# Optimization experiments

Measured on AMD Instinct MI355X. Metric: run time of the kernel, lower is better.

The kernel has to match this reference:

```python
import jax, jax.numpy as jnp
import numpy as np

DT = 0.1
THRESH = 0.01


def setup_inputs() -> dict:
    key = jax.random.key(0)
    ks = jax.random.split(key, 4)
    B, C, H, W = 4, 64, 128, 128
    field = jax.random.normal(ks[0], (B, C, H, W), dtype=jnp.float32)
    # depthwise 3x3 conv weight [C,1,3,3], fan_in = 9
    dw = jax.random.normal(ks[1], (C, 1, 3, 3), dtype=jnp.float32) * (1.0 / 3.0)
    db = jnp.zeros((C,), jnp.float32)
    # 1x1 convs as matrices: w1 [2C, C], w2 [C, 2C]
    w1 = jax.random.normal(ks[2], (2 * C, C), dtype=jnp.float32) * (1.0 / np.sqrt(C))
    b1 = jnp.zeros((2 * C,), jnp.float32)
    w2 = jax.random.normal(ks[3], (C, 2 * C), dtype=jnp.float32) * (1.0 / np.sqrt(2 * C))
    b2 = jnp.zeros((C,), jnp.float32)
    dcoeff = jnp.ones((1,), jnp.float32) * 0.1  # diffusion_coeff init
    return {"field": field, "dw": dw, "db": db, "w1": w1, "b1": b1,
            "w2": w2, "b2": b2, "dcoeff": dcoeff, "max_steps": 50}


def _dynamics(f, dw, db, w1, b1, w2, b2, dcoeff):
    C = f.shape[1]
    diff = jax.lax.conv_general_dilated(
        f, dw, window_strides=(1, 1), padding="SAME",
        feature_group_count=C,
        dimension_numbers=("NCHW", "OIHW", "NCHW")) + db[None, :, None, None]
    h = jax.nn.gelu(jnp.einsum("bchw,oc->bohw", f, w1) + b1[None, :, None, None],
                    approximate=False)
    react = jnp.einsum("bchw,oc->bohw", h, w2) + b2[None, :, None, None]
    return dcoeff[0] * diff + react


def reference(field, dw, db, w1, b1, w2, b2, dcoeff, max_steps):
    def step(carry, _):
        f, done, steps = carry
        deriv = _dynamics(f, dw, db, w1, b1, w2, b2, dcoeff)
        new_f = f + DT * deriv
        change = jnp.mean(jnp.abs(new_f - f))
        f2 = jnp.where(done, f, new_f)          # freeze field once converged
        steps2 = steps + jnp.where(done, 0, 1)  # steps_taken is adaptive
        done2 = done | (change < THRESH)
        return (f2, done2, steps2), None

    init = (field, jnp.asarray(False), jnp.asarray(0, jnp.int32))
    (final_field, _, steps), _ = jax.lax.scan(step, init, None, length=max_steps)
    return final_field, steps
```

## Files before the change

### kernel.cpp

```cpp
#include <hip/hip_runtime.h>
#include <math.h>

#define BATCH 4
#define CCH   64
#define HDIM  128
#define WDIM  128
#define HW    (HDIM * WDIM)
#define NELEM (BATCH * CCH * HW)
#define OCH   128
#define NSTEPS 50
#define NBLK  1024
#define DT 0.1f
#define THRESH 0.01f

typedef short bf16x8 __attribute__((ext_vector_type(8)));
typedef float f32x4  __attribute__((ext_vector_type(4)));

__global__ void init_kernel(double* p0, double* p1, int* stepsvar) {
    int i = blockIdx.x * blockDim.x + threadIdx.x;
    if (i < NBLK) {
        p0[i] = (i == 0) ? 1.0e9 : 0.0;
        p1[i] = 0.0;
    }
    if (i == 0) *stepsvar = 0;
}

__device__ __forceinline__ short f2bf(float x) {
    unsigned u = __float_as_uint(x);
    unsigned r = u + 0x7fff + ((u >> 16) & 1);
    return (short)(r >> 16);
}

__device__ __forceinline__ int pk(float a, float b) {
    return (f2bf(a) & 0xffff) | (((int)f2bf(b)) << 16);
}

__device__ __forceinline__ float bf_lo(int v) { return __int_as_float(v << 16); }
__device__ __forceinline__ float bf_hi(int v) { return __int_as_float(v & 0xffff0000); }

__device__ __forceinline__ float dpp_up1(float v) {
    return __int_as_float(__builtin_amdgcn_update_dpp(
        0, __float_as_int(v), 0x138, 0xf, 0xf, false));
}
__device__ __forceinline__ float dpp_dn1(float v) {
    return __int_as_float(__builtin_amdgcn_update_dpp(
        0, __float_as_int(v), 0x130, 0xf, 0xf, false));
}

__global__ void prep_kernel(const float* __restrict__ w1,
                            const float* __restrict__ w2,
                            short* __restrict__ w1b, short* __restrict__ w2b) {
    int i = blockIdx.x * blockDim.x + threadIdx.x;
    if (i < OCH * CCH) {
        w1b[i] = f2bf(w1[i]);
        w2b[i] = f2bf(w2[i]);
    }
}

__device__ __forceinline__ float gelu_fast(float x) {
    float u  = x * 0.70710678118654752f;
    float au = fabsf(u);
    float t  = __builtin_amdgcn_rcpf(fmaf(0.3275911f, au, 1.0f));
    float p  = fmaf(1.061405429f, t, -1.453152027f);
    p = fmaf(p, t, 1.421413741f);
    p = fmaf(p, t, -0.284496736f);
    p = fmaf(p, t, 0.254829592f);
    p = p * t;
    float ex = __expf(-au * au);
    float e  = fmaf(-p, ex, 1.0f);
    float er = copysignf(e, x);
    return 0.5f * x * (1.0f + er);
}

__global__ __launch_bounds__(256, 4) void step_kernel(
    const float* __restrict__ fin, float* __restrict__ fout,
    const float* __restrict__ dw, const float* __restrict__ db,
    const short* __restrict__ w1b, const float* __restrict__ b1,
    const short* __restrict__ w2b, const float* __restrict__ b2,
    const float* __restrict__ dcoeff,
    const double* __restrict__ pin, double* __restrict__ pout,
    int* __restrict__ stepsvar, int sidx)
{
    const int tid  = threadIdx.x;
    const int lane = tid & 63;
    const int w    = tid >> 6;
    const int quad = (lane >> 4);
    const int lp   = lane & 15;
    const int blk  = blockIdx.x;
    const int xcd  = blk & 7;
    const int idx  = blk >> 3;
    const int y    = xcd * 16 + (idx & 15);
    const int b    = (idx >> 4) & 3;
    const int seg  = idx >> 6;
    const int px0  = seg * 64;
    const int fbase = b * CCH * HW + y * WDIM + px0;

    __shared__ int4   sBf4[64 * 8];
    __shared__ int4   sH4 [64 * 16];
    __shared__ float  sSeam[384];
    __shared__ float  sDw[CCH * 9];
    __shared__ float  sDb[CCH];
    __shared__ double sdred[4];
    __shared__ float  wred[4];
    short* sBf = (short*)sBf4;
    short* sH  = (short*)sH4;
    int*   sRi = (int*)sBf4;

    double ds = pin[tid] + pin[tid + 256] + pin[tid + 512] + pin[tid + 768];
    #pragma unroll
    for (int off = 32; off > 0; off >>= 1) ds += __shfl_down(ds, off, 64);
    if (lane == 0) sdred[w] = ds;

    for (int i = tid; i < CCH * 9; i += 256) sDw[i] = dw[i];
    if (tid < CCH) sDb[tid] = db[tid];

    if (tid < 192) {
        #pragma unroll
        for (int k = 0; k < 2; ++k) {
            int e    = tid * 2 + k;
            int row  = e >> 7;
            int side = (e >> 6) & 1;
            int ch   = e & 63;
            int gy   = y - 1 + row;
            int gx   = px0 + (side ? 64 : -1);
            float v  = 0.0f;
            if (gy >= 0 && gy < HDIM && gx >= 0 && gx < WDIM)
                v = fin[b * CCH * HW + ch * HW + gy * WDIM + gx];
            sSeam[e] = v;
        }
    }

    bf16x8 a1[2][2];
    #pragma unroll
    for (int mt = 0; mt < 2; ++mt)
        #pragma unroll
        for (int kk = 0; kk < 2; ++kk)
            a1[mt][kk] = *(const bf16x8*)(w1b + (w * 32 + mt * 16 + lp) * CCH
                                          + kk * 32 + quad * 8);
    f32x4 b1v[2];
    #pragma unroll
    for (int mt = 0; mt < 2; ++mt)
        b1v[mt] = *(const f32x4*)(b1 + w * 32 + mt * 16 + quad * 4);
    f32x4 b2v = *(const f32x4*)(b2 + w * 16 + quad * 4);

    float f[16];
    {
        #pragma unroll
        for (int i = 0; i < 16; ++i)
            f[i] = fin[fbase + (w * 16 + i) * HW + lane];
        int4 v0, v1;
        v0.x = pk(f[0], f[1]);   v0.y = pk(f[2], f[3]);
        v0.z = pk(f[4], f[5]);   v0.w = pk(f[6], f[7]);
        v1.x = pk(f[8], f[9]);   v1.y = pk(f[10], f[11]);
        v1.z = pk(f[12], f[13]); v1.w = pk(f[14], f[15]);
        int g0 = (w * 2)     ^ (lane & 7);
        int g1 = (w * 2 + 1) ^ (lane & 7);
        sBf4[lane * 8 + g0] = v0;
        sBf4[lane * 8 + g1] = v1;
    }
    __syncthreads();

    {
        double tot = sdred[0] + sdred[1] + sdred[2] + sdred[3];
        if ((float)(tot * (1.0 / (double)NELEM)) < THRESH) {
            if (tid == 0) pout[blk] = pin[blk];
            return;
        }
    }
    if (blk == 0 && tid == 0) *stepsvar = sidx + 1;

    f32x4 acc1[2][4];
    #pragma unroll
    for (int mt = 0; mt < 2; ++mt)
        #pragma unroll
        for (int nt = 0; nt < 4; ++nt)
            acc1[mt][nt] = (f32x4)0.0f;

    #pragma unroll
    for (int kk = 0; kk < 2; ++kk) {
        #pragma unroll
        for (int nt = 0; nt < 4; ++nt) {
            int px = nt * 16 + lp;
            int g  = kk * 4 + quad;
            bf16x8 bfrag = *(const bf16x8*)(sBf + px * 64 + (g ^ (px & 7)) * 8);
            #pragma unroll
            for (int mt = 0; mt < 2; ++mt)
                acc1[mt][nt] = __builtin_amdgcn_mfma_f32_16x16x32_bf16(
                    a1[mt][kk], bfrag, acc1[mt][nt], 0, 0, 0);
        }
    }

    bf16x8 a2[4];
    #pragma unroll
    for (int kk = 0; kk < 4; ++kk)
        a2[kk] = *(const bf16x8*)(w2b + (w * 16 + lp) * OCH + kk * 32 + quad * 8);

    #pragma unroll
    for (int mt = 0; mt < 2; ++mt) {
        #pragma unroll
        for (int nt = 0; nt < 4; ++nt) {
            int px = nt * 16 + lp;
            float h0 = gelu_fast(acc1[mt][nt][0] + b1v[mt][0]);
            float h1 = gelu_fast(acc1[mt][nt][1] + b1v[mt][1]);
            float h2 = gelu_fast(acc1[mt][nt][2] + b1v[mt][2]);
            float h3 = gelu_fast(acc1[mt][nt][3] + b1v[mt][3]);
            int o0  = w * 32 + mt * 16 + quad * 4;
            int g   = o0 >> 3;
            int sub = o0 & 7;
            int gp  = (g & 8) | ((g ^ (px & 7)) & 7);
            int2 hv; hv.x = pk(h0, h1); hv.y = pk(h2, h3);
            *(int2*)(sH + px * 128 + gp * 8 + sub) = hv;
        }
    }

    float hm[16], hp[16];
    {
        const float* fb = fin + fbase + lane;
        if (y > 0) {
            #pragma unroll
            for (int i = 0; i < 16; ++i) hm[i] = fb[(w * 16 + i) * HW - WDIM];
        } else {
            #pragma unroll
            for (int i = 0; i < 16; ++i) hm[i] = 0.0f;
        }
        if (y < HDIM - 1) {
            #pragma unroll
            for (int i = 0; i < 16; ++i) hp[i] = fb[(w * 16 + i) * HW + WDIM];
        } else {
            #pragma unroll
            for (int i = 0; i < 16; ++i) hp[i] = 0.0f;
        }
    }
    __syncthreads();

    f32x4 acc2[4];
    #pragma unroll
    for (int nt = 0; nt < 4; ++nt) acc2[nt] = (f32x4)0.0f;

    #pragma unroll
    for (int kk = 0; kk < 4; ++kk) {
        #pragma unroll
        for (int nt = 0; nt < 4; ++nt) {
            int px = nt * 16 + lp;
            int g  = kk * 4 + quad;
            int gp = (g & 8) | ((g ^ (px & 7)) & 7);
            bf16x8 hfrag = *(const bf16x8*)(sH + px * 128 + gp * 8);
            acc2[nt] = __builtin_amdgcn_mfma_f32_16x16x32_bf16(
                a2[kk], hfrag, acc2[nt], 0, 0, 0);
        }
    }

    #pragma unroll
    for (int nt = 0; nt < 4; ++nt) {
        int px = nt * 16 + lp;
        sRi[(w * 8 + quad * 2 + 0) * 64 + px]
            = pk(acc2[nt][0] + b2v[0], acc2[nt][1] + b2v[1]);
        sRi[(w * 8 + quad * 2 + 1) * 64 + px]
            = pk(acc2[nt][2] + b2v[2], acc2[nt][3] + b2v[3]);
    }
    __syncthreads();

    float react[16];
    #pragma unroll
    for (int ii = 0; ii < 8; ++ii) {
        int v = sRi[(w * 8 + ii) * 64 + lane];
        react[2 * ii]     = bf_lo(v);
        react[2 * ii + 1] = bf_hi(v);
    }

    const float dc = dcoeff[0];
    float csum = 0.0f;

    #pragma unroll
    for (int i = 0; i < 16; ++i) {
        const int c = w * 16 + i;
        const float* wk = sDw + c * 9;
        float vm = hm[i], vc = f[i], vp = hp[i];
        float lm = dpp_up1(vm), lc = dpp_up1(vc), lq = dpp_up1(vp);
        float rm = dpp_dn1(vm), rc = dpp_dn1(vc), rq = dpp_dn1(vp);
        lm = (lane == 0)  ? sSeam[0 * 128 + 0 + c]   : lm;
        lc = (lane == 0)  ? sSeam[1 * 128 + 0 + c]   : lc;
        lq = (lane == 0)  ? sSeam[2 * 128 + 0 + c]   : lq;
        rm = (lane == 63) ? sSeam[0 * 128 + 64 + c]  : rm;
        rc = (lane == 63) ? sSeam[1 * 128 + 64 + c]  : rc;
        rq = (lane == 63) ? sSeam[2 * 128 + 64 + c]  : rq;

        float d = sDb[c];
        d = fmaf(wk[0], lm, d); d = fmaf(wk[1], vm, d); d = fmaf(wk[2], rm, d);
        d = fmaf(wk[3], lc, d); d = fmaf(wk[4], vc, d); d = fmaf(wk[5], rc, d);
        d = fmaf(wk[6], lq, d); d = fmaf(wk[7], vp, d); d = fmaf(wk[8], rq, d);

        float nf = vc + DT * (dc * d + react[i]);
        fout[fbase + c * HW + lane] = nf;
        csum += fabsf(nf - vc);
    }

    float v = csum;
    #pragma unroll
    for (int off = 32; off > 0; off >>= 1) v += __shfl_down(v, off, 64);
    if (lane == 0) wred[w] = v;
    __syncthreads();
    if (tid == 0) {
        pout[blk] = (double)wred[0] + (double)wred[1]
                  + (double)wred[2] + (double)wred[3];
    }
}

__global__ void output_kernel(const float* __restrict__ bufA,
                              float* __restrict__ out,
                              const int* __restrict__ stepsvar)
{
    int i = blockIdx.x * blockDim.x + threadIdx.x;
    int K = *stepsvar;
    bool fromA = (((K - 1) & 1) == 0);
    if (i < NELEM && fromA) out[i] = bufA[i];
    if (i == 0) out[NELEM] = (float)K;
}

extern "C" void kernel_launch(void* const* d_in, const int* in_sizes, int n_in,
                              void* d_out, int out_size, void* d_ws, size_t ws_size,
                              hipStream_t stream)
{
    const float* field  = (const float*)d_in[0];
    const float* dw     = (const float*)d_in[1];
    const float* db     = (const float*)d_in[2];
    const float* w1     = (const float*)d_in[3];
    const float* b1     = (const float*)d_in[4];
    const float* w2     = (const float*)d_in[5];
    const float* b2     = (const float*)d_in[6];
    const float* dcoeff = (const float*)d_in[7];

    float* out = (float*)d_out;

    char* ws = (char*)d_ws;
    float*  bufA = (float*)ws;
    short*  w1b  = (short*)(ws + (size_t)NELEM * 4 + 256);
    short*  w2b  = (short*)(ws + (size_t)NELEM * 4 + 256 + 16384);
    double* P0   = (double*)(ws + (size_t)NELEM * 4 + 256 + 32768);
    double* P1   = P0 + NBLK;
    int* stepsvar = (int*)(P1 + NBLK);

    init_kernel<<<4, 256, 0, stream>>>(P0, P1, stepsvar);
    prep_kernel<<<(OCH * CCH + 255) / 256, 256, 0, stream>>>(w1, w2, w1b, w2b);

    float*  bufs[2]  = { bufA, out };
    double* psums[2] = { P0, P1 };
    const float* fin = field;
    for (int s = 1; s <= NSTEPS; ++s) {
        float* fout = bufs[(s - 1) & 1];
        step_kernel<<<NBLK, 256, 0, stream>>>(
            fin, fout, dw, db, w1b, b1, w2b, b2, dcoeff,
            psums[(s - 1) & 1], psums[s & 1], stepsvar, s - 1);
        fin = fout;
    }

    output_kernel<<<(NELEM + 255) / 256, 256, 0, stream>>>(bufA, out, stepsvar);
}
```

Baseline: 1.046 ms.

## Store intermediate field state in bf16 between time steps

The evolving field is kept in bf16 ping-pong workspace buffers instead of fp32, so each step reads and writes half as many bytes. The first step is a template specialisation that reads the fp32 input, and the output kernel widens the final bf16 state back to fp32. The MFMA operand packing reuses the raw bf16 bits directly. The trade-off is that rounding error now accumulates across the 50 steps, and the stencil, residual update and convergence check all see bf16-rounded values.

```diff
diff --git a/kernel.cpp b/kernel.cpp
--- a/kernel.cpp
+++ b/kernel.cpp
@@ -37,6 +37,7 @@
 
 __device__ __forceinline__ float bf_lo(int v) { return __int_as_float(v << 16); }
 __device__ __forceinline__ float bf_hi(int v) { return __int_as_float(v & 0xffff0000); }
+__device__ __forceinline__ float us2f(int u)  { return __int_as_float(u << 16); }
 
 __device__ __forceinline__ float dpp_up1(float v) {
     return __int_as_float(__builtin_amdgcn_update_dpp(
@@ -72,8 +73,9 @@
     return 0.5f * x * (1.0f + er);
 }
 
+template<bool FIRST>
 __global__ __launch_bounds__(256, 4) void step_kernel(
-    const float* __restrict__ fin, float* __restrict__ fout,
+    const void* __restrict__ finv, unsigned short* __restrict__ fout,
     const float* __restrict__ dw, const float* __restrict__ db,
     const short* __restrict__ w1b, const float* __restrict__ b1,
     const short* __restrict__ w2b, const float* __restrict__ b2,
@@ -81,6 +83,9 @@
     const double* __restrict__ pin, double* __restrict__ pout,
     int* __restrict__ stepsvar, int sidx)
 {
+    const float*          fin32 = (const float*)finv;
+    const unsigned short* fin16 = (const unsigned short*)finv;
+
     const int tid  = threadIdx.x;
     const int lane = tid & 63;
     const int w    = tid >> 6;
@@ -124,8 +129,10 @@
             int gy   = y - 1 + row;
             int gx   = px0 + (side ? 64 : -1);
             float v  = 0.0f;
-            if (gy >= 0 && gy < HDIM && gx >= 0 && gx < WDIM)
-                v = fin[b * CCH * HW + ch * HW + gy * WDIM + gx];
+            if (gy >= 0 && gy < HDIM && gx >= 0 && gx < WDIM) {
+                int gi = b * CCH * HW + ch * HW + gy * WDIM + gx;
+                v = FIRST ? fin32[gi] : us2f(fin16[gi]);
+            }
             sSeam[e] = v;
         }
     }
@@ -145,14 +152,27 @@
 
     float f[16];
     {
-        #pragma unroll
-        for (int i = 0; i < 16; ++i)
-            f[i] = fin[fbase + (w * 16 + i) * HW + lane];
         int4 v0, v1;
-        v0.x = pk(f[0], f[1]);   v0.y = pk(f[2], f[3]);
-        v0.z = pk(f[4], f[5]);   v0.w = pk(f[6], f[7]);
-        v1.x = pk(f[8], f[9]);   v1.y = pk(f[10], f[11]);
-        v1.z = pk(f[12], f[13]); v1.w = pk(f[14], f[15]);
+        if (FIRST) {
+            #pragma unroll
+            for (int i = 0; i < 16; ++i)
+                f[i] = fin32[fbase + (w * 16 + i) * HW + lane];
+            v0.x = pk(f[0], f[1]);   v0.y = pk(f[2], f[3]);
+            v0.z = pk(f[4], f[5]);   v0.w = pk(f[6], f[7]);
+            v1.x = pk(f[8], f[9]);   v1.y = pk(f[10], f[11]);
+            v1.z = pk(f[12], f[13]); v1.w = pk(f[14], f[15]);
+        } else {
+            int u[16];
+            #pragma unroll
+            for (int i = 0; i < 16; ++i) {
+                u[i] = fin16[fbase + (w * 16 + i) * HW + lane];
+                f[i] = us2f(u[i]);
+            }
+            v0.x = u[0] | (u[1] << 16);   v0.y = u[2] | (u[3] << 16);
+            v0.z = u[4] | (u[5] << 16);   v0.w = u[6] | (u[7] << 16);
+            v1.x = u[8] | (u[9] << 16);   v1.y = u[10] | (u[11] << 16);
+            v1.z = u[12] | (u[13] << 16); v1.w = u[14] | (u[15] << 16);
+        }
         int g0 = (w * 2)     ^ (lane & 7);
         int g1 = (w * 2 + 1) ^ (lane & 7);
         sBf4[lane * 8 + g0] = v0;
@@ -215,17 +235,22 @@
 
     float hm[16], hp[16];
     {
-        const float* fb = fin + fbase + lane;
         if (y > 0) {
             #pragma unroll
-            for (int i = 0; i < 16; ++i) hm[i] = fb[(w * 16 + i) * HW - WDIM];
+            for (int i = 0; i < 16; ++i) {
+                int gi = fbase + (w * 16 + i) * HW - WDIM + lane;
+                hm[i] = FIRST ? fin32[gi] : us2f(fin16[gi]);
+            }
         } else {
             #pragma unroll
             for (int i = 0; i < 16; ++i) hm[i] = 0.0f;
         }
         if (y < HDIM - 1) {
             #pragma unroll
-            for (int i = 0; i < 16; ++i) hp[i] = fb[(w * 16 + i) * HW + WDIM];
+            for (int i = 0; i < 16; ++i) {
+                int gi = fbase + (w * 16 + i) * HW + WDIM + lane;
+                hp[i] = FIRST ? fin32[gi] : us2f(fin16[gi]);
+            }
         } else {
             #pragma unroll
             for (int i = 0; i < 16; ++i) hp[i] = 0.0f;
@@ -291,7 +316,7 @@
         d = fmaf(wk[6], lq, d); d = fmaf(wk[7], vp, d); d = fmaf(wk[8], rq, d);
 
         float nf = vc + DT * (dc * d + react[i]);
-        fout[fbase + c * HW + lane] = nf;
+        fout[fbase + c * HW + lane] = (unsigned short)(f2bf(nf) & 0xffff);
         csum += fabsf(nf - vc);
     }
 
@@ -306,14 +331,15 @@
     }
 }
 
-__global__ void output_kernel(const float* __restrict__ bufA,
+__global__ void output_kernel(const unsigned short* __restrict__ G0,
+                              const unsigned short* __restrict__ G1,
                               float* __restrict__ out,
                               const int* __restrict__ stepsvar)
 {
     int i = blockIdx.x * blockDim.x + threadIdx.x;
     int K = *stepsvar;
-    bool fromA = (((K - 1) & 1) == 0);
-    if (i < NELEM && fromA) out[i] = bufA[i];
+    const unsigned short* G = (((K - 1) & 1) == 0) ? G0 : G1;
+    if (i < NELEM) out[i] = __int_as_float(((int)G[i]) << 16);
     if (i == 0) out[NELEM] = (float)K;
 }
 
@@ -333,26 +359,34 @@
     float* out = (float*)d_out;
 
     char* ws = (char*)d_ws;
-    float*  bufA = (float*)ws;
-    short*  w1b  = (short*)(ws + (size_t)NELEM * 4 + 256);
-    short*  w2b  = (short*)(ws + (size_t)NELEM * 4 + 256 + 16384);
-    double* P0   = (double*)(ws + (size_t)NELEM * 4 + 256 + 32768);
+    unsigned short* G0 = (unsigned short*)ws;
+    unsigned short* G1 = G0 + NELEM;
+    char* tail = ws + (size_t)NELEM * 4;
+    short*  w1b  = (short*)(tail + 256);
+    short*  w2b  = (short*)(tail + 256 + 16384);
+    double* P0   = (double*)(tail + 256 + 32768);
     double* P1   = P0 + NBLK;
     int* stepsvar = (int*)(P1 + NBLK);
 
     init_kernel<<<4, 256, 0, stream>>>(P0, P1, stepsvar);
     prep_kernel<<<(OCH * CCH + 255) / 256, 256, 0, stream>>>(w1, w2, w1b, w2b);
 
-    float*  bufs[2]  = { bufA, out };
+    unsigned short* bufs[2] = { G0, G1 };
     double* psums[2] = { P0, P1 };
-    const float* fin = field;
+    const void* fin = (const void*)field;
     for (int s = 1; s <= NSTEPS; ++s) {
-        float* fout = bufs[(s - 1) & 1];
-        step_kernel<<<NBLK, 256, 0, stream>>>(
-            fin, fout, dw, db, w1b, b1, w2b, b2, dcoeff,
-            psums[(s - 1) & 1], psums[s & 1], stepsvar, s - 1);
-        fin = fout;
-    }
-
-    output_kernel<<<(NELEM + 255) / 256, 256, 0, stream>>>(bufA, out, stepsvar);
-}
+        unsigned short* fout = bufs[(s - 1) & 1];
+        if (s == 1) {
+            step_kernel<true><<<NBLK, 256, 0, stream>>>(
+                fin, fout, dw, db, w1b, b1, w2b, b2, dcoeff,
+                psums[(s - 1) & 1], psums[s & 1], stepsvar, s - 1);
+        } else {
+            step_kernel<false><<<NBLK, 256, 0, stream>>>(
+                fin, fout, dw, db, w1b, b1, w2b, b2, dcoeff,
+                psums[(s - 1) & 1], psums[s & 1], stepsvar, s - 1);
+        }
+        fin = (const void*)fout;
+    }
+
+    output_kernel<<<(NELEM + 256) / 256, 256, 0, stream>>>(G0, G1, out, stepsvar);
+}
```

Result: faster. 1.006 ms (-3.8%).
